# Performance work log

Hardware: AMD Instinct MI355X
Metric: run time of the kernel (lower is better)

Reference implementation:

```python
import jax, jax.numpy as jnp
import numpy as np

B, T, C, H = 4096, 4, 1024, 8
DH = C // H
SCALE = DH ** -0.5
LN_EPS = 1e-5


def setup_inputs() -> dict:
    key = jax.random.key(0)
    k1, k2, k3 = jax.random.split(key, 3)
    feats = jax.random.normal(k1, (B, T, C), dtype=jnp.float32)
    Wqkv = jax.random.normal(k2, (T, C, 3 * C), dtype=jnp.float32) * 0.02
    bqkv = jnp.zeros((T, 3 * C), dtype=jnp.float32)
    Wproj = jax.random.normal(k3, (T, C, C), dtype=jnp.float32) * 0.02
    bproj = jnp.zeros((T, C), dtype=jnp.float32)
    gamma = jnp.ones((C,), dtype=jnp.float32)
    beta = jnp.zeros((C,), dtype=jnp.float32)
    return {"feats": feats, "Wqkv": Wqkv, "bqkv": bqkv,
            "Wproj": Wproj, "bproj": bproj, "gamma": gamma, "beta": beta}


def reference(feats, Wqkv, bqkv, Wproj, bproj, gamma, beta):
    # Grouped per-task QKV projection: [B,T,C] x [T,C,3C] -> [B,T,3C]
    qkv = jnp.einsum('btc,tcd->btd', feats, Wqkv) + bqkv
    q, k, v = jnp.split(qkv, 3, axis=-1)           # each [B,T,C]
    q = q.reshape(B, T, H, DH)
    k = k.reshape(B, T, H, DH)
    v = v.reshape(B, T, H, DH)
    # Cross-task attention: scores[b, query_task, key_task, head]
    scores = jnp.einsum('bqhd,bkhd->bqkh', q, k) * SCALE
    attn = jax.nn.softmax(scores, axis=2)          # softmax over key-task dim
    ctx = jnp.einsum('bqkh,bkhd->bqhd', attn, v)   # [B,T,H,DH]
    ctx = ctx.reshape(B, T, C)
    # Grouped per-task output projection (dropout is identity in eval)
    ctx = jnp.einsum('btc,tcd->btd', ctx, Wproj) + bproj
    # Residual + shared LayerNorm over channel dim
    x = ctx + feats
    mu = jnp.mean(x, axis=-1, keepdims=True)
    var = jnp.mean(jnp.square(x - mu), axis=-1, keepdims=True)
    return (x - mu) * jax.lax.rsqrt(var + LN_EPS) * gamma + beta
```

## Files before the change

### kernel.cpp

```cpp
#include <hip/hip_runtime.h>
#include <hip/hip_bf16.h>
#include <cstdint>
#include <cstddef>

#define B_SZ 4096
#define T_SZ 4
#define C_SZ 1024
#define H_SZ 8
#define DH_SZ 128
#define NQKV 3072
#define SCALE_F 0.08838834764831845f

typedef float f32x4 __attribute__((ext_vector_type(4)));
typedef short s16x8 __attribute__((ext_vector_type(8)));

static __device__ __forceinline__ float bf2f(unsigned short u) {
    union { unsigned int i; float f; } x; x.i = ((unsigned int)u) << 16; return x.f;
}
static __device__ __forceinline__ unsigned short f2bf(float f) {
    union { unsigned int i; float f; } x; x.f = f;
    unsigned int r = x.i + 0x7FFFu + ((x.i >> 16) & 1u);
    return (unsigned short)(r >> 16);
}

typedef const __attribute__((address_space(1))) void* gas_ptr;
typedef __attribute__((address_space(3))) void* las_ptr;
static __device__ __forceinline__ void async16(const void* g, void* l) {
    __builtin_amdgcn_global_load_lds((gas_ptr)g, (las_ptr)l, 16, 0, 0);
}

__global__ __launch_bounds__(256) void cvt_f32_bf16(const float* __restrict__ src,
                                                    unsigned short* __restrict__ dst, int n4) {
    int i = blockIdx.x * 256 + threadIdx.x;
    if (i >= n4) return;
    float4 v = reinterpret_cast<const float4*>(src)[i];
    ushort4 o;
    o.x = f2bf(v.x); o.y = f2bf(v.y); o.z = f2bf(v.z); o.w = f2bf(v.w);
    reinterpret_cast<ushort4*>(dst)[i] = o;
}

__global__ __launch_bounds__(256) void transpose_cvt(const float* __restrict__ src,
                                                     unsigned short* __restrict__ dst,
                                                     int K, int N) {
    __shared__ float tile[32][33];
    const float* s = src + (size_t)blockIdx.z * K * N;
    unsigned short* d = dst + (size_t)blockIdx.z * K * N;
    int n0 = blockIdx.x * 32, k0 = blockIdx.y * 32;
    int tx = threadIdx.x, ty = threadIdx.y;
#pragma unroll
    for (int i = 0; i < 4; i++) {
        int k = k0 + ty + i * 8;
        tile[ty + i * 8][tx] = s[(size_t)k * N + n0 + tx];
    }
    __syncthreads();
#pragma unroll
    for (int i = 0; i < 4; i++) {
        int n = n0 + ty + i * 8;
        d[(size_t)n * K + k0 + tx] = f2bf(tile[tx][ty + i * 8]);
    }
}

template<int NSIZE, int EPI>
__global__ __launch_bounds__(256) void gemm_bf16(
    const unsigned short* __restrict__ A,
    const unsigned short* __restrict__ Bt,
    const float* __restrict__ bias,
    const float* __restrict__ resid,
    unsigned short* __restrict__ out_bf,
    float* __restrict__ out_f)
{
    constexpr int BM = 128, BN = 128, BK = 32;
    __shared__ unsigned short lA[BM * BK];
    __shared__ unsigned short lB[BN * BK];

    const int t   = blockIdx.z;
    const int m0  = blockIdx.y * BM;
    const int n0  = blockIdx.x * BN;
    const int tid = threadIdx.x;
    const int lane = tid & 63;
    const int wave = tid >> 6;
    const int wm = (wave >> 1) * 64;
    const int wn = (wave & 1) * 64;
    const int quad = lane >> 4;
    const int l16  = lane & 15;

    const unsigned short* Abase = A + (size_t)t * C_SZ;
    const unsigned short* Bbase = Bt + (size_t)t * NSIZE * C_SZ;

    const int j0 = wave * 2;
    const unsigned short* gA[2];
    const unsigned short* gB[2];
    unsigned short* lAdst[2];
    unsigned short* lBdst[2];
#pragma unroll
    for (int j = 0; j < 2; j++) {
        int slot = (j0 + j) * 64 + lane;
        int row = slot >> 2;
        int ch  = (slot & 3) ^ (row & 3);
        gA[j] = Abase + (size_t)(m0 + row) * (T_SZ * C_SZ) + ch * 8;
        gB[j] = Bbase + (size_t)(n0 + row) * C_SZ + ch * 8;
        lAdst[j] = &lA[(j0 + j) * 512];
        lBdst[j] = &lB[(j0 + j) * 512];
    }

    const int sw = quad ^ (l16 & 3);
    const s16x8* aP[4];
    const s16x8* bP[4];
#pragma unroll
    for (int i = 0; i < 4; i++) {
        aP[i] = reinterpret_cast<const s16x8*>(&lA[(wm + i * 16 + l16) * BK + sw * 8]);
        bP[i] = reinterpret_cast<const s16x8*>(&lB[(wn + i * 16 + l16) * BK + sw * 8]);
    }

    f32x4 acc[4][4] = {};

    for (int kk = 0; kk < C_SZ; kk += BK) {
        async16(gA[0] + kk, lAdst[0]);
        async16(gA[1] + kk, lAdst[1]);
        async16(gB[0] + kk, lBdst[0]);
        async16(gB[1] + kk, lBdst[1]);
        __syncthreads();

        s16x8 af[4], bfr[4];
#pragma unroll
        for (int i = 0; i < 4; i++) { af[i] = *aP[i]; bfr[i] = *bP[i]; }
#pragma unroll
        for (int mi = 0; mi < 4; mi++)
#pragma unroll
            for (int ni = 0; ni < 4; ni++)
                acc[mi][ni] = __builtin_amdgcn_mfma_f32_16x16x32_bf16(
                    af[mi], bfr[ni], acc[mi][ni], 0, 0, 0);
        __syncthreads();
    }

#pragma unroll
    for (int ni = 0; ni < 4; ni++) {
        int gn = n0 + wn + ni * 16 + l16;
        float bi = bias[t * NSIZE + gn];
#pragma unroll
        for (int mi = 0; mi < 4; mi++) {
#pragma unroll
            for (int r = 0; r < 4; r++) {
                int gm = m0 + wm + mi * 16 + quad * 4 + r;
                size_t o = (size_t)(gm * T_SZ + t) * NSIZE + gn;
                float v = acc[mi][ni][r] + bi;
                if (EPI == 0) {
                    out_bf[o] = f2bf(v);
                } else {
                    out_f[o] = v + resid[o];
                }
            }
        }
    }
}

__global__ __launch_bounds__(256) void attn_kernel(const unsigned short* __restrict__ qkv,
                                                   unsigned short* __restrict__ ctx) {
    int wave = threadIdx.x >> 6, lane = threadIdx.x & 63;
    int g = blockIdx.x * 4 + wave;
    int b = g >> 3, h = g & 7;
    int d0 = lane * 2;

    const unsigned short* base = qkv + (size_t)b * T_SZ * NQKV + h * DH_SZ + d0;
    float qf[4][2], kf[4][2], vf[4][2];
#pragma unroll
    for (int i = 0; i < 4; i++) {
        const unsigned short* p = base + (size_t)i * NQKV;
        qf[i][0] = bf2f(p[0]);          qf[i][1] = bf2f(p[1]);
        kf[i][0] = bf2f(p[C_SZ]);       kf[i][1] = bf2f(p[C_SZ + 1]);
        vf[i][0] = bf2f(p[2 * C_SZ]);   vf[i][1] = bf2f(p[2 * C_SZ + 1]);
    }
    float s[4][4];
#pragma unroll
    for (int i = 0; i < 4; i++)
#pragma unroll
        for (int j = 0; j < 4; j++) {
            float p = qf[i][0] * kf[j][0] + qf[i][1] * kf[j][1];
#pragma unroll
            for (int off = 32; off > 0; off >>= 1) p += __shfl_xor(p, off);
            s[i][j] = p * SCALE_F;
        }
#pragma unroll
    for (int i = 0; i < 4; i++) {
        float m = fmaxf(fmaxf(s[i][0], s[i][1]), fmaxf(s[i][2], s[i][3]));
        float e0 = __expf(s[i][0] - m), e1 = __expf(s[i][1] - m);
        float e2 = __expf(s[i][2] - m), e3 = __expf(s[i][3] - m);
        float inv = 1.0f / (e0 + e1 + e2 + e3);
        s[i][0] = e0 * inv; s[i][1] = e1 * inv; s[i][2] = e2 * inv; s[i][3] = e3 * inv;
    }
#pragma unroll
    for (int i = 0; i < 4; i++) {
        float o0 = s[i][0] * vf[0][0] + s[i][1] * vf[1][0] + s[i][2] * vf[2][0] + s[i][3] * vf[3][0];
        float o1 = s[i][0] * vf[0][1] + s[i][1] * vf[1][1] + s[i][2] * vf[2][1] + s[i][3] * vf[3][1];
        size_t o = (size_t)(b * T_SZ + i) * C_SZ + h * DH_SZ + d0;
        ctx[o] = f2bf(o0); ctx[o + 1] = f2bf(o1);
    }
}

__global__ __launch_bounds__(256) void ln_kernel(const float* __restrict__ y,
                                                 const float* __restrict__ gamma,
                                                 const float* __restrict__ beta,
                                                 float* __restrict__ out) {
    int row = blockIdx.x;
    int lane = threadIdx.x & 63, wave = threadIdx.x >> 6;
    float4 v = reinterpret_cast<const float4*>(y + (size_t)row * C_SZ)[threadIdx.x];
    float s  = v.x + v.y + v.z + v.w;
    float ss = v.x * v.x + v.y * v.y + v.z * v.z + v.w * v.w;
#pragma unroll
    for (int off = 32; off > 0; off >>= 1) { s += __shfl_xor(s, off); ss += __shfl_xor(ss, off); }
    __shared__ float red[8];
    if (lane == 0) { red[wave] = s; red[wave + 4] = ss; }
    __syncthreads();
    float S  = red[0] + red[1] + red[2] + red[3];
    float SS = red[4] + red[5] + red[6] + red[7];
    float mean = S * (1.0f / C_SZ);
    float var  = SS * (1.0f / C_SZ) - mean * mean;
    float inv  = rsqrtf(var + 1e-5f);
    float4 g  = reinterpret_cast<const float4*>(gamma)[threadIdx.x];
    float4 be = reinterpret_cast<const float4*>(beta)[threadIdx.x];
    float4 o;
    o.x = (v.x - mean) * inv * g.x + be.x;
    o.y = (v.y - mean) * inv * g.y + be.y;
    o.z = (v.z - mean) * inv * g.z + be.z;
    o.w = (v.w - mean) * inv * g.w + be.w;
    reinterpret_cast<float4*>(out + (size_t)row * C_SZ)[threadIdx.x] = o;
}

extern "C" void kernel_launch(void* const* d_in, const int* in_sizes, int n_in,
                              void* d_out, int out_size, void* d_ws, size_t ws_size,
                              hipStream_t stream) {
    const float* feats = (const float*)d_in[0];
    const float* Wqkv  = (const float*)d_in[1];
    const float* bqkv  = (const float*)d_in[2];
    const float* Wproj = (const float*)d_in[3];
    const float* bproj = (const float*)d_in[4];
    const float* gamma = (const float*)d_in[5];
    const float* beta  = (const float*)d_in[6];
    float* out = (float*)d_out;

    char* ws = (char*)d_ws;
    unsigned short* feats_bf = (unsigned short*)(ws);
    unsigned short* wqkv_t   = (unsigned short*)(ws + 33554432);
    unsigned short* wproj_t  = (unsigned short*)(ws + 58720256);
    unsigned short* qkv      = (unsigned short*)(ws + 67108864);
    unsigned short* ctx      = (unsigned short*)(ws + 167772160);
    float* ybuf              = (float*)(ws + 67108864);

    cvt_f32_bf16<<<16384, 256, 0, stream>>>(feats, feats_bf, (B_SZ * T_SZ * C_SZ) / 4);
    transpose_cvt<<<dim3(96, 32, 4), dim3(32, 8), 0, stream>>>(Wqkv, wqkv_t, C_SZ, NQKV);
    transpose_cvt<<<dim3(32, 32, 4), dim3(32, 8), 0, stream>>>(Wproj, wproj_t, C_SZ, C_SZ);

    gemm_bf16<NQKV, 0><<<dim3(NQKV / 128, B_SZ / 128, T_SZ), 256, 0, stream>>>(
        feats_bf, wqkv_t, bqkv, nullptr, qkv, nullptr);

    attn_kernel<<<(B_SZ * H_SZ) / 4, 256, 0, stream>>>(qkv, ctx);

    gemm_bf16<C_SZ, 1><<<dim3(C_SZ / 128, B_SZ / 128, T_SZ), 256, 0, stream>>>(
        ctx, wproj_t, bproj, feats, nullptr, ybuf);

    ln_kernel<<<B_SZ * T_SZ, 256, 0, stream>>>(ybuf, gamma, beta, out);
}
```

Before: 446.4 us.

## Rewrite grouped GEMMs as 256x256 double-buffered, 8-wave pipelined kernel

Replaces the 128x128 BK=32 single-buffered GEMM with a 256x256 tile, BK=64, 512-thread kernel. It double-buffers LDS through async global-to-LDS loads and interleaves MFMA phases with staged prefetches under explicit barriers, waitcnts and s_setprio. It also adds an XCD-aware block index swizzle over a flat 1-D grid. The aim is to raise data reuse per tile and hide global-load latency behind MFMA work, at the cost of 128KB LDS per block and heavy register use. The 256 blocks of the projection GEMM may underfill the GPU.

```diff
diff --git a/kernel.cpp b/kernel.cpp
--- a/kernel.cpp
+++ b/kernel.cpp
@@ -61,7 +61,7 @@
 }
 
 template<int NSIZE, int EPI>
-__global__ __launch_bounds__(256) void gemm_bf16(
+__global__ __launch_bounds__(512, 2) void gemm256(
     const unsigned short* __restrict__ A,
     const unsigned short* __restrict__ Bt,
     const float* __restrict__ bias,
@@ -69,79 +69,156 @@
     unsigned short* __restrict__ out_bf,
     float* __restrict__ out_f)
 {
-    constexpr int BM = 128, BN = 128, BK = 32;
-    __shared__ unsigned short lA[BM * BK];
-    __shared__ unsigned short lB[BN * BK];
-
-    const int t   = blockIdx.z;
-    const int m0  = blockIdx.y * BM;
-    const int n0  = blockIdx.x * BN;
-    const int tid = threadIdx.x;
+    constexpr int BK  = 64;
+    constexpr int NT  = C_SZ / BK;
+    constexpr int NBX = NSIZE / 256;
+    constexpr int NBY = B_SZ / 256;
+    constexpr int NWG = NBX * NBY * T_SZ;
+
+    __shared__ __align__(16) unsigned short lds[65536];
+
+    const int bid = blockIdx.x;
+    const int swz = (bid & 7) * (NWG >> 3) + (bid >> 3);
+    const int by  = swz & (NBY - 1);
+    const int tmp = swz >> 4;
+    const int bx  = tmp % NBX;
+    const int t   = tmp / NBX;
+    const int m0  = by * 256;
+    const int n0  = bx * 256;
+
+    const int tid  = threadIdx.x;
     const int lane = tid & 63;
-    const int wave = tid >> 6;
-    const int wm = (wave >> 1) * 64;
-    const int wn = (wave & 1) * 64;
+    const int w    = tid >> 6;
+    const int wm   = w >> 2;
+    const int wn   = w & 3;
     const int quad = lane >> 4;
     const int l16  = lane & 15;
 
+    const int q0  = w * 128 + lane;
+    const int q1  = q0 + 64;
+    const int r0  = q0 >> 3, ch0 = (q0 & 7) ^ (r0 & 7);
+    const int r1  = q1 >> 3, ch1 = (q1 & 7) ^ (r1 & 7);
     const unsigned short* Abase = A + (size_t)t * C_SZ;
     const unsigned short* Bbase = Bt + (size_t)t * NSIZE * C_SZ;
-
-    const int j0 = wave * 2;
-    const unsigned short* gA[2];
-    const unsigned short* gB[2];
-    unsigned short* lAdst[2];
-    unsigned short* lBdst[2];
-#pragma unroll
-    for (int j = 0; j < 2; j++) {
-        int slot = (j0 + j) * 64 + lane;
-        int row = slot >> 2;
-        int ch  = (slot & 3) ^ (row & 3);
-        gA[j] = Abase + (size_t)(m0 + row) * (T_SZ * C_SZ) + ch * 8;
-        gB[j] = Bbase + (size_t)(n0 + row) * C_SZ + ch * 8;
-        lAdst[j] = &lA[(j0 + j) * 512];
-        lBdst[j] = &lB[(j0 + j) * 512];
-    }
-
-    const int sw = quad ^ (l16 & 3);
-    const s16x8* aP[4];
-    const s16x8* bP[4];
-#pragma unroll
-    for (int i = 0; i < 4; i++) {
-        aP[i] = reinterpret_cast<const s16x8*>(&lA[(wm + i * 16 + l16) * BK + sw * 8]);
-        bP[i] = reinterpret_cast<const s16x8*>(&lB[(wn + i * 16 + l16) * BK + sw * 8]);
-    }
-
-    f32x4 acc[4][4] = {};
-
-    for (int kk = 0; kk < C_SZ; kk += BK) {
-        async16(gA[0] + kk, lAdst[0]);
-        async16(gA[1] + kk, lAdst[1]);
-        async16(gB[0] + kk, lBdst[0]);
-        async16(gB[1] + kk, lBdst[1]);
-        __syncthreads();
-
-        s16x8 af[4], bfr[4];
-#pragma unroll
-        for (int i = 0; i < 4; i++) { af[i] = *aP[i]; bfr[i] = *bP[i]; }
-#pragma unroll
-        for (int mi = 0; mi < 4; mi++)
-#pragma unroll
-            for (int ni = 0; ni < 4; ni++)
-                acc[mi][ni] = __builtin_amdgcn_mfma_f32_16x16x32_bf16(
-                    af[mi], bfr[ni], acc[mi][ni], 0, 0, 0);
-        __syncthreads();
-    }
-
-#pragma unroll
-    for (int ni = 0; ni < 4; ni++) {
-        int gn = n0 + wn + ni * 16 + l16;
+    const unsigned short* gA0 = Abase + (size_t)(m0 + r0) * (T_SZ * C_SZ) + ch0 * 8;
+    const unsigned short* gA1 = Abase + (size_t)(m0 + r1) * (T_SZ * C_SZ) + ch1 * 8;
+    const unsigned short* gB0 = Bbase + (size_t)(n0 + r0) * C_SZ + ch0 * 8;
+    const unsigned short* gB1 = Bbase + (size_t)(n0 + r1) * C_SZ + ch1 * 8;
+    unsigned short* dA0 = &lds[(w * 2 + 0) * 512];
+    unsigned short* dA1 = &lds[(w * 2 + 1) * 512];
+    unsigned short* dB0 = &lds[32768 + (w * 2 + 0) * 512];
+    unsigned short* dB1 = &lds[32768 + (w * 2 + 1) * 512];
+
+#define STG_A(buf, h, kt) do { \
+    async16(gA0 + (size_t)(h) * 128 * (T_SZ * C_SZ) + (kt) * BK, dA0 + (buf) * 16384 + (h) * 8192); \
+    async16(gA1 + (size_t)(h) * 128 * (T_SZ * C_SZ) + (kt) * BK, dA1 + (buf) * 16384 + (h) * 8192); \
+} while (0)
+#define STG_B(buf, h, kt) do { \
+    async16(gB0 + (size_t)(h) * 128 * C_SZ + (kt) * BK, dB0 + (buf) * 16384 + (h) * 8192); \
+    async16(gB1 + (size_t)(h) * 128 * C_SZ + (kt) * BK, dB1 + (buf) * 16384 + (h) * 8192); \
+} while (0)
+
+    const int s7   = l16 & 7;
+    const int swk0 = ((0 * 4 + quad) ^ s7) * 8;
+    const int swk1 = ((1 * 4 + quad) ^ s7) * 8;
+    const unsigned short* aR = &lds[wm * 8192 + l16 * 64];
+    const unsigned short* bR = &lds[32768 + (wn >> 1) * 8192 + ((wn & 1) * 64 + l16) * 64];
+
+#define LD_A(buf, mh) do { \
+    _Pragma("unroll") \
+    for (int mi = 0; mi < 4; ++mi) { \
+        af[mi][0] = *(const s16x8*)(aR + (buf) * 16384 + ((mh) * 4 + mi) * 1024 + swk0); \
+        af[mi][1] = *(const s16x8*)(aR + (buf) * 16384 + ((mh) * 4 + mi) * 1024 + swk1); \
+    } \
+} while (0)
+#define LD_B(buf, nh, dst) do { \
+    _Pragma("unroll") \
+    for (int ni = 0; ni < 2; ++ni) { \
+        dst[ni][0] = *(const s16x8*)(bR + (buf) * 16384 + ((nh) * 2 + ni) * 1024 + swk0); \
+        dst[ni][1] = *(const s16x8*)(bR + (buf) * 16384 + ((nh) * 2 + ni) * 1024 + swk1); \
+    } \
+} while (0)
+#define MM(mh, nh, bsrc) do { \
+    _Pragma("unroll") \
+    for (int mi = 0; mi < 4; ++mi) \
+    _Pragma("unroll") \
+    for (int ni = 0; ni < 2; ++ni) { \
+        acc[(mh) * 4 + mi][(nh) * 2 + ni] = __builtin_amdgcn_mfma_f32_16x16x32_bf16( \
+            af[mi][0], bsrc[ni][0], acc[(mh) * 4 + mi][(nh) * 2 + ni], 0, 0, 0); \
+        acc[(mh) * 4 + mi][(nh) * 2 + ni] = __builtin_amdgcn_mfma_f32_16x16x32_bf16( \
+            af[mi][1], bsrc[ni][1], acc[(mh) * 4 + mi][(nh) * 2 + ni], 0, 0, 0); \
+    } \
+} while (0)
+#define WAITK() do { \
+    asm volatile("s_waitcnt lgkmcnt(0)"); \
+    __builtin_amdgcn_sched_barrier(0); \
+} while (0)
+#define KTILE(buf, kt, SP0, SP23, VMC) do { \
+     \
+    asm volatile("s_waitcnt vmcnt(" #VMC ")"); \
+    __builtin_amdgcn_sched_barrier(0); \
+    LD_A(buf, 0); LD_B(buf, 0, bq0); \
+    if (SP0) STG_A((buf) ^ 1, 1, (kt) + 1); \
+    __builtin_amdgcn_s_barrier(); \
+    WAITK(); \
+    __builtin_amdgcn_s_setprio(1); MM(0, 0, bq0); __builtin_amdgcn_s_setprio(0); \
+    __builtin_amdgcn_s_barrier(); \
+     \
+    LD_B(buf, 1, bq1); \
+    __builtin_amdgcn_s_barrier(); \
+    WAITK(); \
+    __builtin_amdgcn_s_setprio(1); MM(0, 1, bq1); __builtin_amdgcn_s_setprio(0); \
+    __builtin_amdgcn_s_barrier(); \
+     \
+    LD_A(buf, 1); \
+    if (SP23) { STG_B(buf, 0, (kt) + 2); STG_B(buf, 1, (kt) + 2); } \
+    __builtin_amdgcn_s_barrier(); \
+    WAITK(); \
+    __builtin_amdgcn_s_setprio(1); MM(1, 1, bq1); __builtin_amdgcn_s_setprio(0); \
+    __builtin_amdgcn_s_barrier(); \
+     \
+    if (SP23) STG_A(buf, 0, (kt) + 2); \
+    __builtin_amdgcn_s_barrier(); \
+    WAITK(); \
+    __builtin_amdgcn_s_setprio(1); MM(1, 0, bq0); __builtin_amdgcn_s_setprio(0); \
+    __builtin_amdgcn_s_barrier(); \
+} while (0)
+
+    f32x4 acc[8][4] = {};
+    s16x8 af[4][2], bq0[2][2], bq1[2][2];
+
+    STG_B(0, 0, 0); STG_B(0, 1, 0); STG_A(0, 0, 0); STG_A(0, 1, 0);
+    STG_B(1, 0, 1); STG_B(1, 1, 1); STG_A(1, 0, 1);
+    asm volatile("s_waitcnt vmcnt(6)");
+    __builtin_amdgcn_sched_barrier(0);
+    __builtin_amdgcn_s_barrier();
+
+#pragma clang loop unroll(disable)
+    for (int it = 0; it < 7; ++it) {
+        int kt = it * 2;
+        KTILE(0, kt, 1, 1, 6);
+        KTILE(1, kt + 1, 1, 1, 6);
+    }
+    KTILE(0, 14, 1, 0, 6);
+    KTILE(1, 15, 0, 0, 0);
+
+#undef KTILE
+#undef WAITK
+#undef MM
+#undef LD_B
+#undef LD_A
+#undef STG_B
+#undef STG_A
+
+#pragma unroll
+    for (int ni = 0; ni < 4; ++ni) {
+        int gn = n0 + wn * 64 + ni * 16 + l16;
         float bi = bias[t * NSIZE + gn];
 #pragma unroll
-        for (int mi = 0; mi < 4; mi++) {
-#pragma unroll
-            for (int r = 0; r < 4; r++) {
-                int gm = m0 + wm + mi * 16 + quad * 4 + r;
+        for (int mi = 0; mi < 8; ++mi) {
+#pragma unroll
+            for (int r = 0; r < 4; ++r) {
+                int gm = m0 + wm * 128 + mi * 16 + quad * 4 + r;
                 size_t o = (size_t)(gm * T_SZ + t) * NSIZE + gn;
                 float v = acc[mi][ni][r] + bi;
                 if (EPI == 0) {
@@ -250,12 +327,12 @@
     transpose_cvt<<<dim3(96, 32, 4), dim3(32, 8), 0, stream>>>(Wqkv, wqkv_t, C_SZ, NQKV);
     transpose_cvt<<<dim3(32, 32, 4), dim3(32, 8), 0, stream>>>(Wproj, wproj_t, C_SZ, C_SZ);
 
-    gemm_bf16<NQKV, 0><<<dim3(NQKV / 128, B_SZ / 128, T_SZ), 256, 0, stream>>>(
+    gemm256<NQKV, 0><<<dim3(768), 512, 0, stream>>>(
         feats_bf, wqkv_t, bqkv, nullptr, qkv, nullptr);
 
     attn_kernel<<<(B_SZ * H_SZ) / 4, 256, 0, stream>>>(qkv, ctx);
 
-    gemm_bf16<C_SZ, 1><<<dim3(C_SZ / 128, B_SZ / 128, T_SZ), 256, 0, stream>>>(
+    gemm256<C_SZ, 1><<<dim3(256), 512, 0, stream>>>(
         ctx, wproj_t, bproj, feats, nullptr, ybuf);
 
     ln_kernel<<<B_SZ * T_SZ, 256, 0, stream>>>(ybuf, gamma, beta, out);
```

After: 427.4 us. 1.04x faster.
